# Kernel tuning notes

Measured on AMD Instinct MI355X. Metric: run time of the kernel, lower is better.

Reference implementation:

```python
import jax, jax.numpy as jnp
import numpy as np

B, L = 1, 768
D_MSA, D_PAIR, D_STATE, D_RBF = 256, 128, 16, 64
D_NODE, D_EDGE, L0_OUT = 32, 32, 16
D_MSG = 64
N_L1_IN, N_L1_OUT = 3, 2
NTOTALDOFS = 10
TOP_K = 128
D_HID = 128


def _ln(x):
    m = x.mean(-1, keepdims=True)
    v = ((x - m) ** 2).mean(-1, keepdims=True)
    return (x - m) / jnp.sqrt(v + 1e-5)


def _rbf(D):
    # RoseTTAFold-style gaussian RBF of pairwise distances
    mu = jnp.linspace(2.0, 22.0, D_RBF)
    sigma = (22.0 - 2.0) / D_RBF
    return jnp.exp(-((D[..., None] - mu) / sigma) ** 2)


def setup_inputs() -> dict:
    key = jax.random.key(0)
    ks = jax.random.split(key, 48)
    ki = iter(range(48))

    def lin(shape):
        k = ks[next(ki)]
        return jax.random.normal(k, shape, jnp.float32) / np.sqrt(shape[0]).astype(np.float32)

    inp = {
        'msa': jax.random.normal(ks[next(ki)], (B, 1, L, D_MSA), jnp.float32),
        'pair': jax.random.normal(ks[next(ki)], (B, L, L, D_PAIR), jnp.float32),
        'xyz': jax.random.normal(ks[next(ki)], (B, L, 3, 3), jnp.float32),
        'state': jax.random.normal(ks[next(ki)], (B, L, D_STATE), jnp.float32),
        'idx': jnp.tile(jnp.arange(L)[None, :], (B, 1)),
        'rotation_mask': jnp.zeros((B, L), bool),
        # node/edge embedding
        'W_en': lin((D_MSA + D_STATE, D_NODE)), 'b_en': jnp.zeros((D_NODE,)),
        'Wn1': lin((D_NODE, 2 * D_NODE)), 'bn1': jnp.zeros((2 * D_NODE,)),
        'Wn2': lin((2 * D_NODE, D_NODE)), 'bn2': jnp.zeros((D_NODE,)),
        'W_ee': lin((D_PAIR + D_RBF + 1, D_EDGE)), 'b_ee': jnp.zeros((D_EDGE,)),
        'We1': lin((D_EDGE, 2 * D_EDGE)), 'be1': jnp.zeros((2 * D_EDGE,)),
        'We2': lin((2 * D_EDGE, D_EDGE)), 'be2': jnp.zeros((D_EDGE,)),
        # SE3 message passing
        'Wm1': lin((2 * D_NODE + D_EDGE, D_MSG)), 'bm1': jnp.zeros((D_MSG,)),
        'Wm2': lin((D_MSG, D_NODE + N_L1_OUT + N_L1_OUT * N_L1_IN)),
        'bm2': jnp.zeros((D_NODE + N_L1_OUT + N_L1_OUT * N_L1_IN,)),
        'Wl0': lin((2 * D_NODE, L0_OUT)), 'bl0': jnp.zeros((L0_OUT,)),
        # SCPred
        'Ws0': lin((D_MSA, D_HID)), 'bs0': jnp.zeros((D_HID,)),
        'Wsi': lin((L0_OUT, D_HID)), 'bsi': jnp.zeros((D_HID,)),
        'Wp1': lin((D_HID, D_HID)), 'bp1': jnp.zeros((D_HID,)),
        'Wp2': lin((D_HID, D_HID)), 'bp2': jnp.zeros((D_HID,)),
        'Wp3': lin((D_HID, D_HID)), 'bp3': jnp.zeros((D_HID,)),
        'Wp4': lin((D_HID, D_HID)), 'bp4': jnp.zeros((D_HID,)),
        'Wout': lin((D_HID, 2 * NTOTALDOFS)), 'bout': jnp.zeros((2 * NTOTALDOFS,)),
    }
    return inp


def _forward(msa, pair, xyz, state, idx, rotation_mask,
             W_en, b_en, Wn1, bn1, Wn2, bn2, W_ee, b_ee, We1, be1, We2, be2,
             Wm1, bm1, Wm2, bm2, Wl0, bl0,
             Ws0, bs0, Wsi, bsi, Wp1, bp1, Wp2, bp2, Wp3, bp3, Wp4, bp4, Wout, bout):
    Bb, Ll = msa.shape[0], msa.shape[2]
    seq = _ln(msa[:, 0])                         # (B,L,d_msa)
    pair_n = _ln(pair)
    state_n = _ln(state)

    node = jnp.concatenate([seq, state_n], -1) @ W_en + b_en  # (B,L,32)
    node = node + jax.nn.relu(_ln(node) @ Wn1 + bn1) @ Wn2 + bn2
    node = _ln(node)

    # sequence-separation feature (B,L,L,1)
    off = (idx[:, None, :] - idx[:, :, None]).astype(jnp.float32)
    neighbor = (jnp.sign(off) * jnp.log(jnp.abs(off) + 1.0))[..., None]

    cas = xyz[:, :, 1]                            # (B,L,3) CA coords
    D = jnp.sqrt(jnp.sum((cas[:, :, None] - cas[:, None, :]) ** 2, -1) + 1e-8)
    rbf_feat = _rbf(D)                            # (B,L,L,64)

    edge = jnp.concatenate([pair_n, rbf_feat, neighbor], -1) @ W_ee + b_ee  # (B,L,L,32)
    edge = edge + jax.nn.relu(_ln(edge) @ We1 + be1) @ We2 + be2
    edge = _ln(edge)

    # top-k neighbor graph
    _, nbr = jax.lax.top_k(-D, TOP_K)             # (B,L,K)
    edge_feats = jnp.take_along_axis(edge, nbr[..., None], axis=2)  # (B,L,K,32)
    h_j = jax.vmap(lambda n, i: n[i])(node, nbr)                     # (B,L,K,32)
    x_j = jax.vmap(lambda c, i: c[i])(cas, nbr)                      # (B,L,K,3)
    h_i = jnp.broadcast_to(node[:, :, None, :], h_j.shape)

    # SE3-equivariant message passing (scalar messages + equivariant vector mixing)
    m_in = jnp.concatenate([h_i, h_j, edge_feats], -1)               # (B,L,K,96)
    m = jax.nn.relu(m_in @ Wm1 + bm1) @ Wm2 + bm2                    # (B,L,K,40)
    m_l0 = m[..., :D_NODE].mean(2)                                   # (B,L,32)
    w_edge = m[..., D_NODE:D_NODE + N_L1_OUT]                        # (B,L,K,2)
    w_atom = m[..., D_NODE + N_L1_OUT:].mean(2).reshape(Bb, Ll, N_L1_OUT, N_L1_IN)

    state_out = jnp.concatenate([node, m_l0], -1) @ Wl0 + bl0        # (B,L,16)

    rel = x_j - cas[:, :, None, :]                                   # (B,L,K,3)
    vec_edge = jnp.einsum('blkc,blkd->blcd', w_edge, rel) / TOP_K    # (B,L,2,3)
    l1_feats = xyz - xyz[:, :, 1:2, :]                               # (B,L,3,3)
    vec_atom = jnp.einsum('blca,blad->blcd', w_atom, l1_feats)
    offset = vec_edge + vec_atom                                     # (B,L,2,3)

    T = offset[:, :, 0, :] / 10.0
    R = offset[:, :, 1, :] / 100.0
    Qnorm = jnp.sqrt(1.0 + jnp.sum(R * R, -1))
    qA = 1.0 / Qnorm
    qB, qC, qD = R[..., 0] / Qnorm, R[..., 1] / Qnorm, R[..., 2] / Qnorm
    row0 = jnp.stack([qA*qA+qB*qB-qC*qC-qD*qD, 2*qB*qC-2*qA*qD, 2*qB*qD+2*qA*qC], -1)
    row1 = jnp.stack([2*qB*qC+2*qA*qD, qA*qA-qB*qB+qC*qC-qD*qD, 2*qC*qD-2*qA*qB], -1)
    row2 = jnp.stack([2*qB*qD-2*qA*qC, 2*qC*qD+2*qA*qB, qA*qA-qB*qB-qC*qC+qD*qD], -1)
    Rout = jnp.stack([row0, row1, row2], -2)                         # (B,L,3,3)
    I3 = jnp.broadcast_to(jnp.eye(3, dtype=Rout.dtype), Rout.shape)
    Rout = jnp.where(rotation_mask[:, :, None, None], I3, Rout)

    v = xyz - xyz[:, :, 1:2, :]
    xyz_new = jnp.einsum('blij,blaj->blai', Rout, v) + xyz[:, :, 1:2, :] + T[:, :, None, :]

    # SCPred torsion head
    s0 = _ln(msa[:, 0])
    si_in = _ln(state_out)
    si = s0 @ Ws0 + bs0 + si_in @ Wsi + bsi
    si = si + jax.nn.relu(jax.nn.relu(si) @ Wp1 + bp1) @ Wp2 + bp2
    si = si + jax.nn.relu(jax.nn.relu(si) @ Wp3 + bp3) @ Wp4 + bp4
    alpha = (jax.nn.relu(si) @ Wout + bout).reshape(Bb, Ll, NTOTALDOFS, 2)

    return xyz_new, state_out, alpha


def reference(msa, pair, xyz, state, idx, rotation_mask,
              W_en, b_en, Wn1, bn1, Wn2, bn2, W_ee, b_ee, We1, be1, We2, be2,
              Wm1, bm1, Wm2, bm2, Wl0, bl0,
              Ws0, bs0, Wsi, bsi, Wp1, bp1, Wp2, bp2, Wp3, bp3, Wp4, bp4, Wout, bout):
    return _forward(msa, pair, xyz, state, idx, rotation_mask,
                    W_en, b_en, Wn1, bn1, Wn2, bn2, W_ee, b_ee, We1, be1, We2, be2,
                    Wm1, bm1, Wm2, bm2, Wl0, bl0,
                    Ws0, bs0, Wsi, bsi, Wp1, bp1, Wp2, bp2, Wp3, bp3, Wp4, bp4, Wout, bout)


if __name__ == '__main__':
    out = reference(**setup_inputs())
    print([o.shape for o in out])
```

## Files before the change

kernel.cpp:

```cpp
#include <hip/hip_runtime.h>
#include <hip/hip_bf16.h>

#define LL 768
#define TOPK 128

#define WS_SEQ  0
#define WS_NODE (WS_SEQ + LL*256)
#define WS_NBR  (WS_NODE + LL*32)
#define WS_SOUT (WS_NBR + LL*TOPK)
#define WS_CSEE (WS_SOUT + LL*16)
#define WS_PK   (WS_CSEE + 32)

typedef __attribute__((ext_vector_type(8))) short  bf16x8_t;
typedef __attribute__((ext_vector_type(4))) float  f32x4_t;
typedef __attribute__((ext_vector_type(4))) unsigned u32x4_t;

__device__ __forceinline__ unsigned bfpack(float a, float b) {
  unsigned ua = __float_as_uint(a);
  ua = (ua + 0x7fffu + ((ua >> 16) & 1u)) >> 16;
  unsigned ub = __float_as_uint(b);
  ub = (ub + 0x7fffu + ((ub >> 16) & 1u)) & 0xffff0000u;
  return ua | ub;
}
__device__ __forceinline__ float bflo(unsigned v) { return __uint_as_float(v << 16); }
__device__ __forceinline__ float bfhi(unsigned v) { return __uint_as_float(v & 0xffff0000u); }

__device__ __forceinline__ float block_sum_256(float v, float* red, int t) {
#pragma unroll
  for (int o = 32; o > 0; o >>= 1) v += __shfl_xor(v, o, 64);
  __syncthreads();
  if ((t & 63) == 0) red[t >> 6] = v;
  __syncthreads();
  return red[0] + red[1] + red[2] + red[3];
}
// ... 192 lines not shown
    const int lane6 = t & 63;
    for (int f = t >> 6; f < 34; f += 4) {
      const float* W; int N, krow0, ct;
      if (f < 4)       { W = We1;  N = 64; krow0 = 0;                    ct = f;        }
      else if (f < 8)  { W = We2;  N = 32; krow0 = ((f-4)>>1)*32;        ct = (f-4)&1;  }
      else if (f < 12) { W = Wm1;  N = 64; krow0 = 32;                   ct = f-8;      }
      else if (f < 16) { W = Wm1;  N = 64; krow0 = 64;                   ct = f-12;     }
      else if (f < 22) { W = Wm2;  N = 40; krow0 = ((f-16)/3)*32;        ct = (f-16)%3; }
      else if (f < 30) { W = W_ee; N = 32; krow0 = ((f-22)>>1)*32;       ct = (f-22)&1; }
      else             { W = W_ee; N = 32; krow0 = 128 + ((f-30)>>1)*32; ct = (f-30)&1; }
      const int cc = ct*16 + (lane6 & 15);
      const int kb = krow0 + ((lane6 >> 4) << 3);
#pragma unroll
      for (int d = 0; d < 4; ++d) {
        const int k = kb + 2*d;
        const float lo = (cc < N) ? W[k*N + cc]     : 0.f;
        const float hi = (cc < N) ? W[(k+1)*N + cc] : 0.f;
        pkws[f*256 + lane6*4 + d] = bfpack(lo, hi);
      }
    }
  }
}

__global__ __launch_bounds__(256, 4) void kernC(
    const float* __restrict__ pair, const float* __restrict__ xyz,
    const int* __restrict__ idx, const unsigned char* __restrict__ rmask,
    const float* __restrict__ W_ee, const float* __restrict__ b_ee,
    const float* __restrict__ colsum_ee,
    const float* __restrict__ be1, const float* __restrict__ be2,
    const float* __restrict__ Wm1, const float* __restrict__ bm1,
    const float* __restrict__ bm2,
    const float* __restrict__ Wl0, const float* __restrict__ bl0,
    const float* __restrict__ node, const int* __restrict__ nbr,
    const unsigned* __restrict__ pkws,
    float* __restrict__ soutf, float* __restrict__ out)
{
  const int i = blockIdx.x, t = threadIdx.x;
  const int lane = t & 63;
  const int wv = __builtin_amdgcn_readfirstlane(t >> 6);
  __shared__ unsigned Ab[128][17];
  __shared__ unsigned U[128*33];
  __shared__ unsigned nd[128][17];
  __shared__ int   jl[128];
  __shared__ float Dvv[128], xsepv[128];
  __shared__ float relv[128][3];
  __shared__ float ni[32];
  __shared__ float pmv[64], prsv[64];
  __shared__ float mA[128], sgA[128];
  __shared__ float P2[4][44];
  __shared__ float fin[44];

  if (t < 32) ni[t] = node[i*32 + t];
  {
    const int pp = t >> 1, hh2 = t & 1;
    const int jj = nbr[i*TOPK + pp];
    const float4* nr = (const float4*)(node + jj*32 + hh2*16);
    float4 a0 = nr[0], a1 = nr[1], a2 = nr[2], a3 = nr[3];
    unsigned* dst = &nd[pp][hh2*8];
    dst[0] = bfpack(a0.x, a0.y); dst[1] = bfpack(a0.z, a0.w);
    dst[2] = bfpack(a1.x, a1.y); dst[3] = bfpack(a1.z, a1.w);
    dst[4] = bfpack(a2.x, a2.y); dst[5] = bfpack(a2.z, a2.w);
    dst[6] = bfpack(a3.x, a3.y); dst[7] = bfpack(a3.z, a3.w);
    if (hh2 == 0) {
      jl[pp] = jj;
      const float cix = xyz[i*9+3], ciy = xyz[i*9+4], ciz = xyz[i*9+5];
      const float cjx = xyz[jj*9+3], cjy = xyz[jj*9+4], cjz = xyz[jj*9+5];
      relv[pp][0] = cjx - cix;
      relv[pp][1] = cjy - ciy;
      relv[pp][2] = cjz - ciz;
      const float dx = __fadd_rn(cix, -cjx), dy = __fadd_rn(ciy, -cjy),
                  dz = __fadd_rn(ciz, -cjz);
      Dvv[pp] = sqrtf(__fadd_rn(__fadd_rn(__fadd_rn(__fmul_rn(dx,dx),
                        __fmul_rn(dy,dy)), __fmul_rn(dz,dz)), 1e-8f));
      const float offv = (float)(idx[jj] - idx[i]);
      const float sg = (offv > 0.f) ? 1.f : ((offv < 0.f) ? -1.f : 0.f);
      xsepv[pp] = sg * logf(fabsf(offv) + 1.f);
    }
  }
  __syncthreads();

  unsigned (*pairB)[65] = (unsigned (*)[65])U;
  const f32x4_t fz = {0.f, 0.f, 0.f, 0.f};
  for (int sub = 0; sub < 2; ++sub) {
    {
      const int r = t >> 2, qq = t & 3;
      const float* prow = pair + ((size_t)i*LL + jl[sub*64 + r])*128 + qq*32;
      float s = 0.f, ss = 0.f;
#pragma unroll
      for (int n = 0; n < 8; ++n) {
        float4 v = ((const float4*)prow)[n];
        s  += (v.x + v.y) + (v.z + v.w);
        ss += v.x*v.x + v.y*v.y + v.z*v.z + v.w*v.w;
        pairB[r][qq*16 + n*2]     = bfpack(v.x, v.y);
        pairB[r][qq*16 + n*2 + 1] = bfpack(v.z, v.w);
      }
      s  += __shfl_xor(s, 1);  s  += __shfl_xor(s, 2);
      ss += __shfl_xor(ss, 1); ss += __shfl_xor(ss, 2);
      if (qq == 0) {
        const float pm = s * (1.f/128.f);
        const float pv = ss * (1.f/128.f) - pm*pm;
        pmv[r] = pm; prsv[r] = 1.f / sqrtf(pv + 1e-5f);
      }
    }
    __syncthreads();
    {
      const int col = lane & 15, rg = lane >> 4;
      const int eM = wv*16;
      f32x4_t accP[2] = {fz, fz}, accR[2] = {fz, fz};
#pragma unroll
      for (int ks = 0; ks < 4; ++ks) {
        u32x4_t av;
        const unsigned* rp = &pairB[eM + col][ks*16 + rg*4];
        av.x = rp[0]; av.y = rp[1]; av.z = rp[2]; av.w = rp[3];
        const bf16x8_t af = __builtin_bit_cast(bf16x8_t, av);
#pragma unroll
        for (int ct = 0; ct < 2; ++ct) {
          const u32x4_t bv = ((const u32x4_t*)(pkws + (22 + ks*2 + ct)*256))[lane];
          accP[ct] = __builtin_amdgcn_mfma_f32_16x16x32_bf16(
              af, __builtin_bit_cast(bf16x8_t, bv), accP[ct], 0, 0, 0);
        }
      }
      const float Dv = Dvv[sub*64 + eM + col];
#pragma unroll
      for (int ks = 0; ks < 2; ++ks) {
        u32x4_t av;
#pragma unroll
        for (int d = 0; d < 4; ++d) {
          const int k = ks*32 + rg*8 + 2*d;
          const float mu0 = 2.f + (float)k     * (20.f/63.f);
          const float mu1 = 2.f + (float)(k+1) * (20.f/63.f);
          const float u0 = (Dv - mu0) / 0.3125f;
          const float u1 = (Dv - mu1) / 0.3125f;
          ((unsigned*)&av)[d] = bfpack(expf(-(u0*u0)), expf(-(u1*u1)));
        }
        const bf16x8_t af = __builtin_bit_cast(bf16x8_t, av);
#pragma unroll
        for (int ct = 0; ct < 2; ++ct) {
          const u32x4_t bv = ((const u32x4_t*)(pkws + (30 + ks*2 + ct)*256))[lane];
          accR[ct] = __builtin_amdgcn_mfma_f32_16x16x32_bf16(
              af, __builtin_bit_cast(bf16x8_t, bv), accR[ct], 0, 0, 0);
        }
      }
#pragma unroll
      for (int ct = 0; ct < 2; ++ct) {
        const int ch = ct*16 + col;
        const float cs = colsum_ee[ch];
        const float w3 = W_ee[192*32 + ch];
        const float bb = b_ee[ch];
#pragma unroll
        for (int j = 0; j < 4; ++j) {
          const int eloc = eM + rg*4 + j;
          const int e = sub*64 + eloc;
          const float prs = prsv[eloc], pm = pmv[eloc];
          float v = fmaf(prs, accP[ct][j],
                     fmaf(-prs*pm, cs,
                       fmaf(xsepv[e], w3, bb + accR[ct][j])));
          const float p = __shfl_xor(v, 1);
          if (!(lane & 1)) Ab[e][ct*8 + (col >> 1)] = bfpack(v, p);
        }
      }
    }
    __syncthreads();
  }

  unsigned (*Bb)[33] = (unsigned (*)[33])U;
  {
    const int e0b = 32 * wv;
    const int row = lane & 15;
    const int kg  = lane >> 4;
    const int r0  = kg * 4;

    {
      const int eL = e0b + (lane & 31);
      const int hf = lane >> 5;
      float av[16];
#pragma unroll
      for (int kk = 0; kk < 8; ++kk) {
        const unsigned v = Ab[eL][hf*8 + kk];
        av[2*kk] = bflo(v); av[2*kk+1] = bfhi(v);
      }
      float s = 0.f;
#pragma unroll
      for (int c = 0; c < 16; ++c) s += av[c];
      s += __shfl_xor(s, 32);
      const float mm = s * (1.f/32.f);
      float vv = 0.f;
#pragma unroll
      for (int c = 0; c < 16; ++c) { const float dd = av[c] - mm; vv += dd*dd; }
      vv += __shfl_xor(vv, 32);
      vv *= (1.f/32.f);
      const float sg = sqrtf(vv + 1e-5f);
      const float rs = 1.f / sg;
#pragma unroll
      for (int kk = 0; kk < 8; ++kk)
        Ab[eL][hf*8 + kk] = bfpack((av[2*kk]-mm)*rs, (av[2*kk+1]-mm)*rs);
      if (hf == 0) { mA[eL] = mm; sgA[eL] = sg; }
    }

    {
      f32x4_t acc[2][4];
#pragma unroll
      for (int m = 0; m < 2; ++m) {
        u32x4_t av4;
        const unsigned* rp = &Ab[e0b + 16*m + row][0];
        av4.x = rp[kg*4]; av4.y = rp[kg*4+1]; av4.z = rp[kg*4+2]; av4.w = rp[kg*4+3];
        const bf16x8_t af = __builtin_bit_cast(bf16x8_t, av4);
#pragma unroll
        for (int ct = 0; ct < 4; ++ct) {
          const u32x4_t bv = ((const u32x4_t*)(pkws + (0 + ct)*256))[lane];
          acc[m][ct] = __builtin_amdgcn_mfma_f32_16x16x32_bf16(
              af, __builtin_bit_cast(bf16x8_t, bv), fz, 0, 0, 0);
        }
      }
#pragma unroll
      for (int m = 0; m < 2; ++m)
#pragma unroll
        for (int ct = 0; ct < 4; ++ct) {
          const int ch = ct*16 + row;
#pragma unroll
          for (int j = 0; j < 4; ++j) {
            float v = fmaxf(acc[m][ct][j] + be1[ch], 0.f);
            const float p = __shfl_xor(v, 1);
            if (!(lane & 1))
              Bb[e0b + 16*m + r0 + j][ct*8 + (row >> 1)] = bfpack(v, p);
          }
        }
    }

    {
      f32x4_t acc[2][2];
#pragma unroll
      for (int m = 0; m < 2; ++m)
#pragma unroll
        for (int ct = 0; ct < 2; ++ct) acc[m][ct] = fz;
#pragma unroll
      for (int m = 0; m < 2; ++m)
#pragma unroll
        for (int ks = 0; ks < 2; ++ks) {
          u32x4_t av4;
          const unsigned* rp = &Bb[e0b + 16*m + row][0];
          const int kd = ks*16 + kg*4;
          av4.x = rp[kd]; av4.y = rp[kd+1]; av4.z = rp[kd+2]; av4.w = rp[kd+3];
          const bf16x8_t af = __builtin_bit_cast(bf16x8_t, av4);
#pragma unroll
          for (int ct = 0; ct < 2; ++ct) {
            const u32x4_t bv = ((const u32x4_t*)(pkws + (4 + ks*2 + ct)*256))[lane];
            acc[m][ct] = __builtin_amdgcn_mfma_f32_16x16x32_bf16(
                af, __builtin_bit_cast(bf16x8_t, bv), acc[m][ct], 0, 0, 0);
          }
        }
#pragma unroll
      for (int m = 0; m < 2; ++m)
#pragma unroll
        for (int ct = 0; ct < 2; ++ct) {
          const int ch = ct*16 + row;
          const int dw = ct*8 + (row >> 1);
#pragma unroll
          for (int j = 0; j < 4; ++j) {
            const int e = e0b + 16*m + r0 + j;
            const unsigned old = Ab[e][dw];
            const float e0v = (lane & 1) ? bfhi(old) : bflo(old);
            float v = acc[m][ct][j] + fmaf(e0v, sgA[e], mA[e]) + be2[ch];
            const float p = __shfl_xor(v, 1);
            if (!(lane & 1)) Ab[e][dw] = bfpack(v, p);
          }
        }
    }

    {
      const int eL = e0b + (lane & 31);
      const int hf = lane >> 5;
      float av[16];
#pragma unroll
      for (int kk = 0; kk < 8; ++kk) {
        const unsigned v = Ab[eL][hf*8 + kk];
        av[2*kk] = bflo(v); av[2*kk+1] = bfhi(v);
      }
      float s = 0.f;
#pragma unroll
      for (int c = 0; c < 16; ++c) s += av[c];
      s += __shfl_xor(s, 32);
      const float mm = s * (1.f/32.f);
      float vv = 0.f;
#pragma unroll
      for (int c = 0; c < 16; ++c) { const float dd = av[c] - mm; vv += dd*dd; }
      vv += __shfl_xor(vv, 32);
      vv *= (1.f/32.f);
      const float rs = 1.f / sqrtf(vv + 1e-5f);
#pragma unroll
      for (int kk = 0; kk < 8; ++kk)
        Ab[eL][hf*8 + kk] = bfpack((av[2*kk]-mm)*rs, (av[2*kk+1]-mm)*rs);
    }

    {
      float tmpni = bm1[lane];
      for (int k = 0; k < 32; ++k) tmpni = fmaf(ni[k], Wm1[k*64 + lane], tmpni);
      f32x4_t acc[2][4];
#pragma unroll
      for (int m = 0; m < 2; ++m)
#pragma unroll
        for (int ct = 0; ct < 4; ++ct) acc[m][ct] = fz;
#pragma unroll
      for (int m = 0; m < 2; ++m) {
        u32x4_t aN, aE;
        const unsigned* rn = &nd[e0b + 16*m + row][0];
        aN.x = rn[kg*4]; aN.y = rn[kg*4+1]; aN.z = rn[kg*4+2]; aN.w = rn[kg*4+3];
        const unsigned* ra = &Ab[e0b + 16*m + row][0];
        aE.x = ra[kg*4]; aE.y = ra[kg*4+1]; aE.z = ra[kg*4+2]; aE.w = ra[kg*4+3];
        const bf16x8_t afN = __builtin_bit_cast(bf16x8_t, aN);
        const bf16x8_t afE = __builtin_bit_cast(bf16x8_t, aE);
#pragma unroll
        for (int ct = 0; ct < 4; ++ct) {
          const u32x4_t bN = ((const u32x4_t*)(pkws + (8 + ct)*256))[lane];
          const u32x4_t bE = ((const u32x4_t*)(pkws + (12 + ct)*256))[lane];
          acc[m][ct] = __builtin_amdgcn_mfma_f32_16x16x32_bf16(
              afN, __builtin_bit_cast(bf16x8_t, bN), acc[m][ct], 0, 0, 0);
          acc[m][ct] = __builtin_amdgcn_mfma_f32_16x16x32_bf16(
              afE, __builtin_bit_cast(bf16x8_t, bE), acc[m][ct], 0, 0, 0);
        }
      }
#pragma unroll
      for (int m = 0; m < 2; ++m)
#pragma unroll
        for (int ct = 0; ct < 4; ++ct) {
          const int ch = ct*16 + row;
          const float tb = __shfl(tmpni, ch);
#pragma unroll
          for (int j = 0; j < 4; ++j) {
            float v = fmaxf(acc[m][ct][j] + tb, 0.f);
            const float p = __shfl_xor(v, 1);
            if (!(lane & 1))
              Bb[e0b + 16*m + r0 + j][ct*8 + (row >> 1)] = bfpack(v, p);
          }
        }
    }

    {
      f32x4_t acc[2][3];
#pragma unroll
      for (int m = 0; m < 2; ++m)
#pragma unroll
        for (int ct = 0; ct < 3; ++ct) acc[m][ct] = fz;
#pragma unroll
      for (int m = 0; m < 2; ++m)
#pragma unroll
        for (int ks = 0; ks < 2; ++ks) {
          u32x4_t av4;
          const unsigned* rp = &Bb[e0b + 16*m + row][0];
          const int kd = ks*16 + kg*4;
          av4.x = rp[kd]; av4.y = rp[kd+1]; av4.z = rp[kd+2]; av4.w = rp[kd+3];
          const bf16x8_t af = __builtin_bit_cast(bf16x8_t, av4);
#pragma unroll
          for (int ct = 0; ct < 3; ++ct) {
            const u32x4_t bv = ((const u32x4_t*)(pkws + (16 + ks*3 + ct)*256))[lane];
            acc[m][ct] = __builtin_amdgcn_mfma_f32_16x16x32_bf16(
                af, __builtin_bit_cast(bf16x8_t, bv), acc[m][ct], 0, 0, 0);
          }
        }
      float plain[3] = {0.f, 0.f, 0.f};
      float rel3[3]  = {0.f, 0.f, 0.f};
#pragma unroll
      for (int m = 0; m < 2; ++m)
#pragma unroll
        for (int ct = 0; ct < 3; ++ct) {
          const int o = ct*16 + row;
          if (ct == 2 && row >= 8) continue;
#pragma unroll
          for (int j = 0; j < 4; ++j) {
            const int e = e0b + 16*m + r0 + j;
            const float v = acc[m][ct][j] + bm2[o];
            if (ct == 2 && row < 2) {
              rel3[0] = fmaf(v, relv[e][0], rel3[0]);
              rel3[1] = fmaf(v, relv[e][1], rel3[1]);
              rel3[2] = fmaf(v, relv[e][2], rel3[2]);
            } else {
              plain[ct] += v;
            }
          }
        }
#pragma unroll
      for (int d = 0; d < 3; ++d) {
        plain[d] += __shfl_xor(plain[d], 16); plain[d] += __shfl_xor(plain[d], 32);
        rel3[d]  += __shfl_xor(rel3[d], 16);  rel3[d]  += __shfl_xor(rel3[d], 32);
      }
      if (lane < 16) {
        P2[wv][lane]      = plain[0];
        P2[wv][16 + lane] = plain[1];
        if (lane < 2) {
#pragma unroll
          for (int d = 0; d < 3; ++d) P2[wv][32 + lane*3 + d] = rel3[d];
        } else if (lane < 8) {
          P2[wv][38 + lane - 2] = plain[2];
        }
      }
    }
  }
  __syncthreads();
  if (t < 44) fin[t] = P2[0][t] + P2[1][t] + P2[2][t] + P2[3][t];
  __syncthreads();

  if (t < 16) {
    float a = bl0[t];
#pragma unroll
    for (int k = 0; k < 32; ++k) a = fmaf(ni[k], Wl0[k*16 + t], a);
#pragma unroll
    for (int k = 0; k < 32; ++k) a = fmaf(fin[k] * (1.f/128.f), Wl0[(32+k)*16 + t], a);
    soutf[i*16 + t] = a;
    out[LL*9 + i*16 + t] = a;
  }
  if (t == 0) {
    float ve[6], wa[6];
#pragma unroll
    for (int qq = 0; qq < 6; ++qq) ve[qq] = fin[32 + qq] * (1.f/128.f);
#pragma unroll
    for (int qq = 0; qq < 6; ++qq) wa[qq] = fin[38 + qq] * (1.f/128.f);
    float l1[9];
#pragma unroll
    for (int a = 0; a < 3; ++a)
#pragma unroll
      for (int d = 0; d < 3; ++d) l1[a*3 + d] = xyz[i*9 + a*3 + d] - xyz[i*9 + 3 + d];
    float T[3], Rv[3];
#pragma unroll
    for (int d = 0; d < 3; ++d) {
      float va0 = wa[0]*l1[d] + wa[1]*l1[3 + d] + wa[2]*l1[6 + d];
      float va1 = wa[3]*l1[d] + wa[4]*l1[3 + d] + wa[5]*l1[6 + d];
      T[d]  = (ve[d] + va0) / 10.f;
      Rv[d] = (ve[3 + d] + va1) / 100.f;
    }
    float qn = sqrtf(1.f + Rv[0]*Rv[0] + Rv[1]*Rv[1] + Rv[2]*Rv[2]);
    float qA = 1.f/qn, qB = Rv[0]/qn, qC = Rv[1]/qn, qD = Rv[2]/qn;
    float Rm[9];
    Rm[0] = qA*qA + qB*qB - qC*qC - qD*qD;
    Rm[1] = 2.f*qB*qC - 2.f*qA*qD;
    Rm[2] = 2.f*qB*qD + 2.f*qA*qC;
    Rm[3] = 2.f*qB*qC + 2.f*qA*qD;
    Rm[4] = qA*qA - qB*qB + qC*qC - qD*qD;
    Rm[5] = 2.f*qC*qD - 2.f*qA*qB;
    Rm[6] = 2.f*qB*qD - 2.f*qA*qC;
    Rm[7] = 2.f*qC*qD + 2.f*qA*qB;
    Rm[8] = qA*qA - qB*qB - qC*qC + qD*qD;
    if (rmask[i]) {
      Rm[0] = 1.f; Rm[1] = 0.f; Rm[2] = 0.f;
      Rm[3] = 0.f; Rm[4] = 1.f; Rm[5] = 0.f;
      Rm[6] = 0.f; Rm[7] = 0.f; Rm[8] = 1.f;
    }
#pragma unroll
    for (int a = 0; a < 3; ++a)
#pragma unroll
      for (int di = 0; di < 3; ++di) {
        float xn = Rm[di*3+0]*l1[a*3+0] + Rm[di*3+1]*l1[a*3+1] + Rm[di*3+2]*l1[a*3+2]
                 + xyz[i*9 + 3 + di] + T[di];
        out[i*9 + a*3 + di] = xn;
      }
  }
}

__global__ __launch_bounds__(512) void kernD(
    const float* __restrict__ seq_ln, const float* __restrict__ st_out,
    const float* __restrict__ Ws0, const float* __restrict__ bs0,
    const float* __restrict__ Wsi, const float* __restrict__ bsi,
    const float* __restrict__ Wp1, const float* __restrict__ bp1,
    const float* __restrict__ Wp2, const float* __restrict__ bp2,
    const float* __restrict__ Wp3, const float* __restrict__ bp3,
    const float* __restrict__ Wp4, const float* __restrict__ bp4,
    const float* __restrict__ Wout, const float* __restrict__ bout,
    float* __restrict__ out)
{
  const int i = blockIdx.x, t = threadIdx.x;
  const int c = t & 127, g = t >> 7;
  __shared__ float x0[256], stn[16], act[128], resid[128], part[4][129];

  if (t < 256) x0[t] = seq_ln[i*256 + t];
  if (t < 16) {
    float m = 0.f;
    for (int k = 0; k < 16; ++k) m += st_out[i*16 + k];
    m *= (1.f/16.f);
    float v = 0.f;
    for (int k = 0; k < 16; ++k) { float dd = st_out[i*16 + k] - m; v += dd*dd; }
    v *= (1.f/16.f);
    stn[t] = (st_out[i*16 + t] - m) / sqrtf(v + 1e-5f);
  }
  __syncthreads();

  {
    float p = 0.f;
    for (int k = g*64; k < g*64 + 64; ++k) p = fmaf(x0[k], Ws0[k*128 + c], p);
    if (g == 0)
      for (int k = 0; k < 16; ++k) p = fmaf(stn[k], Wsi[k*128 + c], p);
    part[g][c] = p;
  }
  __syncthreads();
  if (t < 128) {
    const float si = part[0][t] + part[1][t] + part[2][t] + part[3][t]
                   + bs0[t] + bsi[t];
    resid[t] = si;
    act[t] = fmaxf(si, 0.f);
  }
  __syncthreads();

  {
    float p = 0.f;
    for (int k = g*32; k < g*32 + 32; ++k) p = fmaf(act[k], Wp1[k*128 + c], p);
    part[g][c] = p;
// ... 71 lines not shown
  const float* Wm2  = (const float*)d_in[20];
  const float* bm2  = (const float*)d_in[21];
  const float* Wl0  = (const float*)d_in[22];
  const float* bl0  = (const float*)d_in[23];
  const float* Ws0  = (const float*)d_in[24];
  const float* bs0  = (const float*)d_in[25];
  const float* Wsi  = (const float*)d_in[26];
  const float* bsi  = (const float*)d_in[27];
  const float* Wp1  = (const float*)d_in[28];
  const float* bp1  = (const float*)d_in[29];
  const float* Wp2  = (const float*)d_in[30];
  const float* bp2  = (const float*)d_in[31];
  const float* Wp3  = (const float*)d_in[32];
  const float* bp3  = (const float*)d_in[33];
  const float* Wp4  = (const float*)d_in[34];
  const float* bp4  = (const float*)d_in[35];
  const float* Wout = (const float*)d_in[36];
  const float* bout = (const float*)d_in[37];

  float* wsf    = (float*)d_ws;
  float* seq_ln = wsf + WS_SEQ;
  float* nodev  = wsf + WS_NODE;
  int*   nbr    = (int*)(wsf + WS_NBR);
  float* soutf  = wsf + WS_SOUT;
  float* csee   = wsf + WS_CSEE;
  unsigned* pkws = (unsigned*)(wsf + WS_PK);
  float* out = (float*)d_out;

  kernABP<<<2*LL + 1, 256, 0, stream>>>(msa, state, W_en, b_en, Wn1, bn1, Wn2, bn2,
                                        xyz, W_ee, We1, We2, Wm1, Wm2,
                                        seq_ln, nodev, nbr, csee, pkws);
  kernC<<<LL, 256, 0, stream>>>(pair, xyz, idx, rmask, W_ee, b_ee, csee,
                                be1, be2, Wm1, bm1, bm2,
                                Wl0, bl0, nodev, nbr, pkws, soutf, out);
  kernD<<<LL, 512, 0, stream>>>(seq_ln, soutf, Ws0, bs0, Wsi, bsi, Wp1, bp1, Wp2, bp2,
                                Wp3, bp3, Wp4, bp4, Wout, bout, out);
}
```

Before: 81.73 us.

## Split kernC neighbor work across two blocks per residue and move finalization into kernD

kernC now runs two blocks per residue, each handling 64 of the 128 neighbors. Each block writes its partial message sums to a workspace buffer, and the per-residue state/xyz finalization moves into kernD, which adds the two partials. This doubles the grid, shrinks shared memory per block and raises the occupancy hint to 5, which should hide latency of the pair gathers better. The cost is an extra global round trip for the partials, and the per-block node-load and setup work is now duplicated.

New measurement: 73.96 us. -9.5%, faster.

```diff
diff --git a/kernel.cpp b/kernel.cpp
--- a/kernel.cpp
+++ b/kernel.cpp
@@ -7,9 +7,9 @@
 #define WS_SEQ  0
 #define WS_NODE (WS_SEQ + LL*256)
 #define WS_NBR  (WS_NODE + LL*32)
-#define WS_SOUT (WS_NBR + LL*TOPK)
-#define WS_CSEE (WS_SOUT + LL*16)
-#define WS_PK   (WS_CSEE + 32)
+#define WS_CSEE (WS_NBR + LL*TOPK)
+#define WS_FIN  (WS_CSEE + 32)
+#define WS_PK   (WS_FIN + LL*2*44)
 
 typedef __attribute__((ext_vector_type(8))) short  bf16x8_t;
 typedef __attribute__((ext_vector_type(4))) float  f32x4_t;
@@ -248,38 +248,35 @@
   }
 }
 
-__global__ __launch_bounds__(256, 4) void kernC(
+__global__ __launch_bounds__(256, 5) void kernC(
     const float* __restrict__ pair, const float* __restrict__ xyz,
-    const int* __restrict__ idx, const unsigned char* __restrict__ rmask,
+    const int* __restrict__ idx,
     const float* __restrict__ W_ee, const float* __restrict__ b_ee,
     const float* __restrict__ colsum_ee,
     const float* __restrict__ be1, const float* __restrict__ be2,
     const float* __restrict__ Wm1, const float* __restrict__ bm1,
     const float* __restrict__ bm2,
-    const float* __restrict__ Wl0, const float* __restrict__ bl0,
     const float* __restrict__ node, const int* __restrict__ nbr,
-    const unsigned* __restrict__ pkws,
-    float* __restrict__ soutf, float* __restrict__ out)
+    const unsigned* __restrict__ pkws, float* __restrict__ fin2)
 {
-  const int i = blockIdx.x, t = threadIdx.x;
-  const int lane = t & 63;
+  const int i = blockIdx.x >> 1, part = blockIdx.x & 1;
+  const int t = threadIdx.x, lane = t & 63;
   const int wv = __builtin_amdgcn_readfirstlane(t >> 6);
-  __shared__ unsigned Ab[128][17];
-  __shared__ unsigned U[128*33];
-  __shared__ unsigned nd[128][17];
-  __shared__ int   jl[128];
-  __shared__ float Dvv[128], xsepv[128];
-  __shared__ float relv[128][3];
+  __shared__ unsigned Ab[64][17];
+  __shared__ unsigned U[64*65];
+  __shared__ unsigned nd[64][17];
+  __shared__ int   jl[64];
+  __shared__ float Dvv[64], xsepv[64];
+  __shared__ float relv[64][3];
   __shared__ float ni[32];
   __shared__ float pmv[64], prsv[64];
-  __shared__ float mA[128], sgA[128];
+  __shared__ float mA[64], sgA[64];
   __shared__ float P2[4][44];
-  __shared__ float fin[44];
 
   if (t < 32) ni[t] = node[i*32 + t];
-  {
+  if (t < 128) {
     const int pp = t >> 1, hh2 = t & 1;
-    const int jj = nbr[i*TOPK + pp];
+    const int jj = nbr[i*TOPK + part*64 + pp];
     const float4* nr = (const float4*)(node + jj*32 + hh2*16);
     float4 a0 = nr[0], a1 = nr[1], a2 = nr[2], a3 = nr[3];
     unsigned* dst = &nd[pp][hh2*8];
@@ -306,304 +303,271 @@
   __syncthreads();
 
   unsigned (*pairB)[65] = (unsigned (*)[65])U;
+  {
+    const int r = t >> 2, qq = t & 3;
+    const float* prow = pair + ((size_t)i*LL + jl[r])*128 + qq*32;
+    float s = 0.f, ss = 0.f;
+#pragma unroll
+    for (int n = 0; n < 8; ++n) {
+      float4 v = ((const float4*)prow)[n];
+      s  += (v.x + v.y) + (v.z + v.w);
+      ss += v.x*v.x + v.y*v.y + v.z*v.z + v.w*v.w;
+      pairB[r][qq*16 + n*2]     = bfpack(v.x, v.y);
+      pairB[r][qq*16 + n*2 + 1] = bfpack(v.z, v.w);
+    }
+    s  += __shfl_xor(s, 1);  s  += __shfl_xor(s, 2);
+    ss += __shfl_xor(ss, 1); ss += __shfl_xor(ss, 2);
+    if (qq == 0) {
+      const float pm = s * (1.f/128.f);
+      const float pv = ss * (1.f/128.f) - pm*pm;
+      pmv[r] = pm; prsv[r] = 1.f / sqrtf(pv + 1e-5f);
+    }
+  }
+  __syncthreads();
+
   const f32x4_t fz = {0.f, 0.f, 0.f, 0.f};
-  for (int sub = 0; sub < 2; ++sub) {
-    {
-      const int r = t >> 2, qq = t & 3;
-      const float* prow = pair + ((size_t)i*LL + jl[sub*64 + r])*128 + qq*32;
-      float s = 0.f, ss = 0.f;
-#pragma unroll
-      for (int n = 0; n < 8; ++n) {
-        float4 v = ((const float4*)prow)[n];
-        s  += (v.x + v.y) + (v.z + v.w);
-        ss += v.x*v.x + v.y*v.y + v.z*v.z + v.w*v.w;
-        pairB[r][qq*16 + n*2]     = bfpack(v.x, v.y);
-        pairB[r][qq*16 + n*2 + 1] = bfpack(v.z, v.w);
-      }
-      s  += __shfl_xor(s, 1);  s  += __shfl_xor(s, 2);
-      ss += __shfl_xor(ss, 1); ss += __shfl_xor(ss, 2);
-      if (qq == 0) {
-        const float pm = s * (1.f/128.f);
-        const float pv = ss * (1.f/128.f) - pm*pm;
-        pmv[r] = pm; prsv[r] = 1.f / sqrtf(pv + 1e-5f);
-      }
-    }
-    __syncthreads();
-    {
-      const int col = lane & 15, rg = lane >> 4;
-      const int eM = wv*16;
-      f32x4_t accP[2] = {fz, fz}, accR[2] = {fz, fz};
-#pragma unroll
-      for (int ks = 0; ks < 4; ++ks) {
-        u32x4_t av;
-        const unsigned* rp = &pairB[eM + col][ks*16 + rg*4];
-        av.x = rp[0]; av.y = rp[1]; av.z = rp[2]; av.w = rp[3];
-        const bf16x8_t af = __builtin_bit_cast(bf16x8_t, av);
-#pragma unroll
-        for (int ct = 0; ct < 2; ++ct) {
-          const u32x4_t bv = ((const u32x4_t*)(pkws + (22 + ks*2 + ct)*256))[lane];
-          accP[ct] = __builtin_amdgcn_mfma_f32_16x16x32_bf16(
-              af, __builtin_bit_cast(bf16x8_t, bv), accP[ct], 0, 0, 0);
-        }
-      }
-      const float Dv = Dvv[sub*64 + eM + col];
-#pragma unroll
-      for (int ks = 0; ks < 2; ++ks) {
-        u32x4_t av;
-#pragma unroll
-        for (int d = 0; d < 4; ++d) {
-          const int k = ks*32 + rg*8 + 2*d;
-          const float mu0 = 2.f + (float)k     * (20.f/63.f);
-          const float mu1 = 2.f + (float)(k+1) * (20.f/63.f);
-          const float u0 = (Dv - mu0) / 0.3125f;
-          const float u1 = (Dv - mu1) / 0.3125f;
-          ((unsigned*)&av)[d] = bfpack(expf(-(u0*u0)), expf(-(u1*u1)));
-        }
-        const bf16x8_t af = __builtin_bit_cast(bf16x8_t, av);
-#pragma unroll
-        for (int ct = 0; ct < 2; ++ct) {
-          const u32x4_t bv = ((const u32x4_t*)(pkws + (30 + ks*2 + ct)*256))[lane];
-          accR[ct] = __builtin_amdgcn_mfma_f32_16x16x32_bf16(
-              af, __builtin_bit_cast(bf16x8_t, bv), accR[ct], 0, 0, 0);
-        }
-      }
+
+  {
+    const int col = lane & 15, rg = lane >> 4;
+    const int eM = wv*16;
+    f32x4_t accP[2] = {fz, fz}, accR[2] = {fz, fz};
+#pragma unroll
+    for (int ks = 0; ks < 4; ++ks) {
+      u32x4_t av;
+      const unsigned* rp = &pairB[eM + col][ks*16 + rg*4];
+      av.x = rp[0]; av.y = rp[1]; av.z = rp[2]; av.w = rp[3];
+      const bf16x8_t af = __builtin_bit_cast(bf16x8_t, av);
 #pragma unroll
       for (int ct = 0; ct < 2; ++ct) {
-        const int ch = ct*16 + col;
-        const float cs = colsum_ee[ch];
-        const float w3 = W_ee[192*32 + ch];
-        const float bb = b_ee[ch];
-#pragma unroll
-        for (int j = 0; j < 4; ++j) {
-          const int eloc = eM + rg*4 + j;
-          const int e = sub*64 + eloc;
-          const float prs = prsv[eloc], pm = pmv[eloc];
-          float v = fmaf(prs, accP[ct][j],
-                     fmaf(-prs*pm, cs,
-                       fmaf(xsepv[e], w3, bb + accR[ct][j])));
-          const float p = __shfl_xor(v, 1);
-          if (!(lane & 1)) Ab[e][ct*8 + (col >> 1)] = bfpack(v, p);
-        }
-      }
-    }
-    __syncthreads();
-  }
+        const u32x4_t bv = ((const u32x4_t*)(pkws + (22 + ks*2 + ct)*256))[lane];
+        accP[ct] = __builtin_amdgcn_mfma_f32_16x16x32_bf16(
+            af, __builtin_bit_cast(bf16x8_t, bv), accP[ct], 0, 0, 0);
+      }
+    }
+    const float Dv = Dvv[eM + col];
+#pragma unroll
+    for (int ks = 0; ks < 2; ++ks) {
+      u32x4_t av;
+#pragma unroll
+      for (int d = 0; d < 4; ++d) {
+        const int k = ks*32 + rg*8 + 2*d;
+        const float mu0 = 2.f + (float)k     * (20.f/63.f);
+        const float mu1 = 2.f + (float)(k+1) * (20.f/63.f);
+        const float u0 = (Dv - mu0) / 0.3125f;
+        const float u1 = (Dv - mu1) / 0.3125f;
+        ((unsigned*)&av)[d] = bfpack(expf(-(u0*u0)), expf(-(u1*u1)));
+      }
+      const bf16x8_t af = __builtin_bit_cast(bf16x8_t, av);
+#pragma unroll
+      for (int ct = 0; ct < 2; ++ct) {
+        const u32x4_t bv = ((const u32x4_t*)(pkws + (30 + ks*2 + ct)*256))[lane];
+        accR[ct] = __builtin_amdgcn_mfma_f32_16x16x32_bf16(
+            af, __builtin_bit_cast(bf16x8_t, bv), accR[ct], 0, 0, 0);
+      }
+    }
+#pragma unroll
+    for (int ct = 0; ct < 2; ++ct) {
+      const int ch = ct*16 + col;
+      const float cs = colsum_ee[ch];
+      const float w3 = W_ee[192*32 + ch];
+      const float bb = b_ee[ch];
+#pragma unroll
+      for (int j = 0; j < 4; ++j) {
+        const int e = eM + rg*4 + j;
+        const float prs = prsv[e], pm = pmv[e];
+        float v = fmaf(prs, accP[ct][j],
+                   fmaf(-prs*pm, cs,
+                     fmaf(xsepv[e], w3, bb + accR[ct][j])));
+        const float p = __shfl_xor(v, 1);
+        if (!(lane & 1)) Ab[e][ct*8 + (col >> 1)] = bfpack(v, p);
+      }
+    }
+  }
+  __syncthreads();
 
   unsigned (*Bb)[33] = (unsigned (*)[33])U;
   {
-    const int e0b = 32 * wv;
+    const int e0b = 16 * wv;
     const int row = lane & 15;
     const int kg  = lane >> 4;
     const int r0  = kg * 4;
 
     {
-      const int eL = e0b + (lane & 31);
-      const int hf = lane >> 5;
-      float av[16];
-#pragma unroll
-      for (int kk = 0; kk < 8; ++kk) {
-        const unsigned v = Ab[eL][hf*8 + kk];
+      const int eL = e0b + row;
+      float av[8];
+#pragma unroll
+      for (int kk = 0; kk < 4; ++kk) {
+        const unsigned v = Ab[eL][kg*4 + kk];
         av[2*kk] = bflo(v); av[2*kk+1] = bfhi(v);
       }
       float s = 0.f;
 #pragma unroll
-      for (int c = 0; c < 16; ++c) s += av[c];
-      s += __shfl_xor(s, 32);
+      for (int c = 0; c < 8; ++c) s += av[c];
+      s += __shfl_xor(s, 16); s += __shfl_xor(s, 32);
       const float mm = s * (1.f/32.f);
       float vv = 0.f;
 #pragma unroll
-      for (int c = 0; c < 16; ++c) { const float dd = av[c] - mm; vv += dd*dd; }
-      vv += __shfl_xor(vv, 32);
+      for (int c = 0; c < 8; ++c) { const float dd = av[c] - mm; vv += dd*dd; }
+      vv += __shfl_xor(vv, 16); vv += __shfl_xor(vv, 32);
       vv *= (1.f/32.f);
       const float sg = sqrtf(vv + 1e-5f);
       const float rs = 1.f / sg;
 #pragma unroll
-      for (int kk = 0; kk < 8; ++kk)
-        Ab[eL][hf*8 + kk] = bfpack((av[2*kk]-mm)*rs, (av[2*kk+1]-mm)*rs);
-      if (hf == 0) { mA[eL] = mm; sgA[eL] = sg; }
+      for (int kk = 0; kk < 4; ++kk)
+        Ab[eL][kg*4 + kk] = bfpack((av[2*kk]-mm)*rs, (av[2*kk+1]-mm)*rs);
+      if (kg == 0) { mA[eL] = mm; sgA[eL] = sg; }
     }
 
     {
-      f32x4_t acc[2][4];
-#pragma unroll
-      for (int m = 0; m < 2; ++m) {
+      u32x4_t av4;
+      const unsigned* rp = &Ab[e0b + row][0];
+      av4.x = rp[kg*4]; av4.y = rp[kg*4+1]; av4.z = rp[kg*4+2]; av4.w = rp[kg*4+3];
+      const bf16x8_t af = __builtin_bit_cast(bf16x8_t, av4);
+      f32x4_t acc[4];
+#pragma unroll
+      for (int ct = 0; ct < 4; ++ct) {
+        const u32x4_t bv = ((const u32x4_t*)(pkws + (0 + ct)*256))[lane];
+        acc[ct] = __builtin_amdgcn_mfma_f32_16x16x32_bf16(
+            af, __builtin_bit_cast(bf16x8_t, bv), fz, 0, 0, 0);
+      }
+#pragma unroll
+      for (int ct = 0; ct < 4; ++ct) {
+        const int ch = ct*16 + row;
+#pragma unroll
+        for (int j = 0; j < 4; ++j) {
+          float v = fmaxf(acc[ct][j] + be1[ch], 0.f);
+          const float p = __shfl_xor(v, 1);
+          if (!(lane & 1))
+            Bb[e0b + r0 + j][ct*8 + (row >> 1)] = bfpack(v, p);
+        }
+      }
+    }
+
+    {
+      f32x4_t acc[2] = {fz, fz};
+#pragma unroll
+      for (int ks = 0; ks < 2; ++ks) {
         u32x4_t av4;
-        const unsigned* rp = &Ab[e0b + 16*m + row][0];
-        av4.x = rp[kg*4]; av4.y = rp[kg*4+1]; av4.z = rp[kg*4+2]; av4.w = rp[kg*4+3];
+        const unsigned* rp = &Bb[e0b + row][0];
+        const int kd = ks*16 + kg*4;
+        av4.x = rp[kd]; av4.y = rp[kd+1]; av4.z = rp[kd+2]; av4.w = rp[kd+3];
         const bf16x8_t af = __builtin_bit_cast(bf16x8_t, av4);
 #pragma unroll
-        for (int ct = 0; ct < 4; ++ct) {
-          const u32x4_t bv = ((const u32x4_t*)(pkws + (0 + ct)*256))[lane];
-          acc[m][ct] = __builtin_amdgcn_mfma_f32_16x16x32_bf16(
-              af, __builtin_bit_cast(bf16x8_t, bv), fz, 0, 0, 0);
+        for (int ct = 0; ct < 2; ++ct) {
+          const u32x4_t bv = ((const u32x4_t*)(pkws + (4 + ks*2 + ct)*256))[lane];
+          acc[ct] = __builtin_amdgcn_mfma_f32_16x16x32_bf16(
+              af, __builtin_bit_cast(bf16x8_t, bv), acc[ct], 0, 0, 0);
         }
       }
 #pragma unroll
-      for (int m = 0; m < 2; ++m)
-#pragma unroll
-        for (int ct = 0; ct < 4; ++ct) {
-          const int ch = ct*16 + row;
-#pragma unroll
-          for (int j = 0; j < 4; ++j) {
-            float v = fmaxf(acc[m][ct][j] + be1[ch], 0.f);
-            const float p = __shfl_xor(v, 1);
-            if (!(lane & 1))
-              Bb[e0b + 16*m + r0 + j][ct*8 + (row >> 1)] = bfpack(v, p);
-          }
+      for (int ct = 0; ct < 2; ++ct) {
+        const int ch = ct*16 + row;
+        const int dw = ct*8 + (row >> 1);
+#pragma unroll
+        for (int j = 0; j < 4; ++j) {
+          const int e = e0b + r0 + j;
+          const unsigned old = Ab[e][dw];
+          const float e0v = (lane & 1) ? bfhi(old) : bflo(old);
+          float v = acc[ct][j] + fmaf(e0v, sgA[e], mA[e]) + be2[ch];
+          const float p = __shfl_xor(v, 1);
+          if (!(lane & 1)) Ab[e][dw] = bfpack(v, p);
         }
+      }
     }
 
     {
-      f32x4_t acc[2][2];
-#pragma unroll
-      for (int m = 0; m < 2; ++m)
-#pragma unroll
-        for (int ct = 0; ct < 2; ++ct) acc[m][ct] = fz;
-#pragma unroll
-      for (int m = 0; m < 2; ++m)
-#pragma unroll
-        for (int ks = 0; ks < 2; ++ks) {
-          u32x4_t av4;
-          const unsigned* rp = &Bb[e0b + 16*m + row][0];
-          const int kd = ks*16 + kg*4;
-          av4.x = rp[kd]; av4.y = rp[kd+1]; av4.z = rp[kd+2]; av4.w = rp[kd+3];
-          const bf16x8_t af = __builtin_bit_cast(bf16x8_t, av4);
-#pragma unroll
-          for (int ct = 0; ct < 2; ++ct) {
-            const u32x4_t bv = ((const u32x4_t*)(pkws + (4 + ks*2 + ct)*256))[lane];
-            acc[m][ct] = __builtin_amdgcn_mfma_f32_16x16x32_bf16(
-                af, __builtin_bit_cast(bf16x8_t, bv), acc[m][ct], 0, 0, 0);
-          }
-        }
-#pragma unroll
-      for (int m = 0; m < 2; ++m)
-#pragma unroll
-        for (int ct = 0; ct < 2; ++ct) {
-          const int ch = ct*16 + row;
-          const int dw = ct*8 + (row >> 1);
-#pragma unroll
-          for (int j = 0; j < 4; ++j) {
-            const int e = e0b + 16*m + r0 + j;
-            const unsigned old = Ab[e][dw];
-            const float e0v = (lane & 1) ? bfhi(old) : bflo(old);
-            float v = acc[m][ct][j] + fmaf(e0v, sgA[e], mA[e]) + be2[ch];
-            const float p = __shfl_xor(v, 1);
-            if (!(lane & 1)) Ab[e][dw] = bfpack(v, p);
-          }
-        }
-    }
-
-    {
-      const int eL = e0b + (lane & 31);
-      const int hf = lane >> 5;
-      float av[16];
-#pragma unroll
-      for (int kk = 0; kk < 8; ++kk) {
-        const unsigned v = Ab[eL][hf*8 + kk];
+      const int eL = e0b + row;
+      float av[8];
+#pragma unroll
+      for (int kk = 0; kk < 4; ++kk) {
+        const unsigned v = Ab[eL][kg*4 + kk];
         av[2*kk] = bflo(v); av[2*kk+1] = bfhi(v);
       }
       float s = 0.f;
 #pragma unroll
-      for (int c = 0; c < 16; ++c) s += av[c];
-      s += __shfl_xor(s, 32);
+      for (int c = 0; c < 8; ++c) s += av[c];
+      s += __shfl_xor(s, 16); s += __shfl_xor(s, 32);
       const float mm = s * (1.f/32.f);
       float vv = 0.f;
 #pragma unroll
-      for (int c = 0; c < 16; ++c) { const float dd = av[c] - mm; vv += dd*dd; }
-      vv += __shfl_xor(vv, 32);
+      for (int c = 0; c < 8; ++c) { const float dd = av[c] - mm; vv += dd*dd; }
+      vv += __shfl_xor(vv, 16); vv += __shfl_xor(vv, 32);
       vv *= (1.f/32.f);
       const float rs = 1.f / sqrtf(vv + 1e-5f);
 #pragma unroll
-      for (int kk = 0; kk < 8; ++kk)
-        Ab[eL][hf*8 + kk] = bfpack((av[2*kk]-mm)*rs, (av[2*kk+1]-mm)*rs);
+      for (int kk = 0; kk < 4; ++kk)
+        Ab[eL][kg*4 + kk] = bfpack((av[2*kk]-mm)*rs, (av[2*kk+1]-mm)*rs);
     }
 
     {
       float tmpni = bm1[lane];
       for (int k = 0; k < 32; ++k) tmpni = fmaf(ni[k], Wm1[k*64 + lane], tmpni);
-      f32x4_t acc[2][4];
-#pragma unroll
-      for (int m = 0; m < 2; ++m)
-#pragma unroll
-        for (int ct = 0; ct < 4; ++ct) acc[m][ct] = fz;
-#pragma unroll
-      for (int m = 0; m < 2; ++m) {
-        u32x4_t aN, aE;
-        const unsigned* rn = &nd[e0b + 16*m + row][0];
-        aN.x = rn[kg*4]; aN.y = rn[kg*4+1]; aN.z = rn[kg*4+2]; aN.w = rn[kg*4+3];
-        const unsigned* ra = &Ab[e0b + 16*m + row][0];
-        aE.x = ra[kg*4]; aE.y = ra[kg*4+1]; aE.z = ra[kg*4+2]; aE.w = ra[kg*4+3];
-        const bf16x8_t afN = __builtin_bit_cast(bf16x8_t, aN);
-        const bf16x8_t afE = __builtin_bit_cast(bf16x8_t, aE);
-#pragma unroll
-        for (int ct = 0; ct < 4; ++ct) {
-          const u32x4_t bN = ((const u32x4_t*)(pkws + (8 + ct)*256))[lane];
-          const u32x4_t bE = ((const u32x4_t*)(pkws + (12 + ct)*256))[lane];
-          acc[m][ct] = __builtin_amdgcn_mfma_f32_16x16x32_bf16(
-              afN, __builtin_bit_cast(bf16x8_t, bN), acc[m][ct], 0, 0, 0);
-          acc[m][ct] = __builtin_amdgcn_mfma_f32_16x16x32_bf16(
-              afE, __builtin_bit_cast(bf16x8_t, bE), acc[m][ct], 0, 0, 0);
+      u32x4_t aN, aE;
+      const unsigned* rn = &nd[e0b + row][0];
+      aN.x = rn[kg*4]; aN.y = rn[kg*4+1]; aN.z = rn[kg*4+2]; aN.w = rn[kg*4+3];
+      const unsigned* ra = &Ab[e0b + row][0];
+      aE.x = ra[kg*4]; aE.y = ra[kg*4+1]; aE.z = ra[kg*4+2]; aE.w = ra[kg*4+3];
+      const bf16x8_t afN = __builtin_bit_cast(bf16x8_t, aN);
+      const bf16x8_t afE = __builtin_bit_cast(bf16x8_t, aE);
+      f32x4_t acc[4];
+#pragma unroll
+      for (int ct = 0; ct < 4; ++ct) {
+        const u32x4_t bN = ((const u32x4_t*)(pkws + (8 + ct)*256))[lane];
+        const u32x4_t bE = ((const u32x4_t*)(pkws + (12 + ct)*256))[lane];
+        acc[ct] = __builtin_amdgcn_mfma_f32_16x16x32_bf16(
+            afN, __builtin_bit_cast(bf16x8_t, bN), fz, 0, 0, 0);
+        acc[ct] = __builtin_amdgcn_mfma_f32_16x16x32_bf16(
+            afE, __builtin_bit_cast(bf16x8_t, bE), acc[ct], 0, 0, 0);
+      }
+#pragma unroll
+      for (int ct = 0; ct < 4; ++ct) {
+        const int ch = ct*16 + row;
+        const float tb = __shfl(tmpni, ch);
+#pragma unroll
+        for (int j = 0; j < 4; ++j) {
+          float v = fmaxf(acc[ct][j] + tb, 0.f);
+          const float p = __shfl_xor(v, 1);
+          if (!(lane & 1))
+            Bb[e0b + r0 + j][ct*8 + (row >> 1)] = bfpack(v, p);
         }
       }
-#pragma unroll
-      for (int m = 0; m < 2; ++m)
-#pragma unroll
-        for (int ct = 0; ct < 4; ++ct) {
-          const int ch = ct*16 + row;
-          const float tb = __shfl(tmpni, ch);
-#pragma unroll
-          for (int j = 0; j < 4; ++j) {
-            float v = fmaxf(acc[m][ct][j] + tb, 0.f);
-            const float p = __shfl_xor(v, 1);
-            if (!(lane & 1))
-              Bb[e0b + 16*m + r0 + j][ct*8 + (row >> 1)] = bfpack(v, p);
+    }
+
+    {
+      f32x4_t acc[3] = {fz, fz, fz};
+#pragma unroll
+      for (int ks = 0; ks < 2; ++ks) {
+        u32x4_t av4;
+        const unsigned* rp = &Bb[e0b + row][0];
+        const int kd = ks*16 + kg*4;
+        av4.x = rp[kd]; av4.y = rp[kd+1]; av4.z = rp[kd+2]; av4.w = rp[kd+3];
+        const bf16x8_t af = __builtin_bit_cast(bf16x8_t, av4);
+#pragma unroll
+        for (int ct = 0; ct < 3; ++ct) {
+          const u32x4_t bv = ((const u32x4_t*)(pkws + (16 + ks*3 + ct)*256))[lane];
+          acc[ct] = __builtin_amdgcn_mfma_f32_16x16x32_bf16(
+              af, __builtin_bit_cast(bf16x8_t, bv), acc[ct], 0, 0, 0);
+        }
+      }
+      float plain[3] = {0.f, 0.f, 0.f};
+      float rel3[3]  = {0.f, 0.f, 0.f};
+#pragma unroll
+      for (int ct = 0; ct < 3; ++ct) {
+        const int o = ct*16 + row;
+        if (ct == 2 && row >= 8) continue;
+#pragma unroll
+        for (int j = 0; j < 4; ++j) {
+          const int e = e0b + r0 + j;
+          const float v = acc[ct][j] + bm2[o];
+          if (ct == 2 && row < 2) {
+            rel3[0] = fmaf(v, relv[e][0], rel3[0]);
+            rel3[1] = fmaf(v, relv[e][1], rel3[1]);
+            rel3[2] = fmaf(v, relv[e][2], rel3[2]);
+          } else {
+            plain[ct] += v;
           }
         }
-    }
-
-    {
-      f32x4_t acc[2][3];
-#pragma unroll
-      for (int m = 0; m < 2; ++m)
-#pragma unroll
-        for (int ct = 0; ct < 3; ++ct) acc[m][ct] = fz;
-#pragma unroll
-      for (int m = 0; m < 2; ++m)
-#pragma unroll
-        for (int ks = 0; ks < 2; ++ks) {
-          u32x4_t av4;
-          const unsigned* rp = &Bb[e0b + 16*m + row][0];
-          const int kd = ks*16 + kg*4;
-          av4.x = rp[kd]; av4.y = rp[kd+1]; av4.z = rp[kd+2]; av4.w = rp[kd+3];
-          const bf16x8_t af = __builtin_bit_cast(bf16x8_t, av4);
-#pragma unroll
-          for (int ct = 0; ct < 3; ++ct) {
-            const u32x4_t bv = ((const u32x4_t*)(pkws + (16 + ks*3 + ct)*256))[lane];
-            acc[m][ct] = __builtin_amdgcn_mfma_f32_16x16x32_bf16(
-                af, __builtin_bit_cast(bf16x8_t, bv), acc[m][ct], 0, 0, 0);
-          }
-        }
-      float plain[3] = {0.f, 0.f, 0.f};
-      float rel3[3]  = {0.f, 0.f, 0.f};
-#pragma unroll
-      for (int m = 0; m < 2; ++m)
-#pragma unroll
-        for (int ct = 0; ct < 3; ++ct) {
-          const int o = ct*16 + row;
-          if (ct == 2 && row >= 8) continue;
-#pragma unroll
-          for (int j = 0; j < 4; ++j) {
-            const int e = e0b + 16*m + r0 + j;
-            const float v = acc[m][ct][j] + bm2[o];
-            if (ct == 2 && row < 2) {
-              rel3[0] = fmaf(v, relv[e][0], rel3[0]);
-              rel3[1] = fmaf(v, relv[e][1], rel3[1]);
-              rel3[2] = fmaf(v, relv[e][2], rel3[2]);
-            } else {
-              plain[ct] += v;
-            }
-          }
-        }
+      }
 #pragma unroll
       for (int d = 0; d < 3; ++d) {
         plain[d] += __shfl_xor(plain[d], 16); plain[d] += __shfl_xor(plain[d], 32);
@@ -622,19 +586,45 @@
     }
   }
   __syncthreads();
-  if (t < 44) fin[t] = P2[0][t] + P2[1][t] + P2[2][t] + P2[3][t];
+  if (t < 44)
+    fin2[(size_t)(i*2 + part)*44 + t] = P2[0][t] + P2[1][t] + P2[2][t] + P2[3][t];
+}
+
+__global__ __launch_bounds__(512) void kernD(
+    const float* __restrict__ seq_ln, const float* __restrict__ xyz,
+    const unsigned char* __restrict__ rmask,
+    const float* __restrict__ Wl0, const float* __restrict__ bl0,
+    const float* __restrict__ node, const float* __restrict__ fin2,
+    const float* __restrict__ Ws0, const float* __restrict__ bs0,
+    const float* __restrict__ Wsi, const float* __restrict__ bsi,
+    const float* __restrict__ Wp1, const float* __restrict__ bp1,
+    const float* __restrict__ Wp2, const float* __restrict__ bp2,
+    const float* __restrict__ Wp3, const float* __restrict__ bp3,
+    const float* __restrict__ Wp4, const float* __restrict__ bp4,
+    const float* __restrict__ Wout, const float* __restrict__ bout,
+    float* __restrict__ out)
+{
+  const int i = blockIdx.x, t = threadIdx.x;
+  const int c = t & 127, g = t >> 7;
+  __shared__ float fin[44], niD[32], sout_s[16], stn[16];
+  __shared__ float x0[256], act[128], resid[128], part[4][129];
+
+  if (t < 44) fin[t] = fin2[(size_t)(i*2)*44 + t] + fin2[(size_t)(i*2+1)*44 + t];
+  if (t >= 64 && t < 96) niD[t-64] = node[i*32 + (t-64)];
+  if (t >= 256) x0[t-256] = seq_ln[i*256 + (t-256)];
+  else if (t >= 128) x0[t] = seq_ln[i*256 + t];
   __syncthreads();
 
   if (t < 16) {
     float a = bl0[t];
 #pragma unroll
-    for (int k = 0; k < 32; ++k) a = fmaf(ni[k], Wl0[k*16 + t], a);
+    for (int k = 0; k < 32; ++k) a = fmaf(niD[k], Wl0[k*16 + t], a);
 #pragma unroll
     for (int k = 0; k < 32; ++k) a = fmaf(fin[k] * (1.f/128.f), Wl0[(32+k)*16 + t], a);
-    soutf[i*16 + t] = a;
+    sout_s[t] = a;
     out[LL*9 + i*16 + t] = a;
   }
-  if (t == 0) {
+  if (t == 32) {
     float ve[6], wa[6];
 #pragma unroll
     for (int qq = 0; qq < 6; ++qq) ve[qq] = fin[32 + qq] * (1.f/128.f);
@@ -679,32 +669,16 @@
         out[i*9 + a*3 + di] = xn;
       }
   }
-}
-
-__global__ __launch_bounds__(512) void kernD(
-    const float* __restrict__ seq_ln, const float* __restrict__ st_out,
-    const float* __restrict__ Ws0, const float* __restrict__ bs0,
-    const float* __restrict__ Wsi, const float* __restrict__ bsi,
-    const float* __restrict__ Wp1, const float* __restrict__ bp1,
-    const float* __restrict__ Wp2, const float* __restrict__ bp2,
-    const float* __restrict__ Wp3, const float* __restrict__ bp3,
-    const float* __restrict__ Wp4, const float* __restrict__ bp4,
-    const float* __restrict__ Wout, const float* __restrict__ bout,
-    float* __restrict__ out)
-{
-  const int i = blockIdx.x, t = threadIdx.x;
-  const int c = t & 127, g = t >> 7;
-  __shared__ float x0[256], stn[16], act[128], resid[128], part[4][129];
-
-  if (t < 256) x0[t] = seq_ln[i*256 + t];
+  __syncthreads();
+
   if (t < 16) {
     float m = 0.f;
-    for (int k = 0; k < 16; ++k) m += st_out[i*16 + k];
+    for (int k = 0; k < 16; ++k) m += sout_s[k];
     m *= (1.f/16.f);
     float v = 0.f;
-    for (int k = 0; k < 16; ++k) { float dd = st_out[i*16 + k] - m; v += dd*dd; }
+    for (int k = 0; k < 16; ++k) { float dd = sout_s[k] - m; v += dd*dd; }
     v *= (1.f/16.f);
-    stn[t] = (st_out[i*16 + t] - m) / sqrtf(v + 1e-5f);
+    stn[t] = (sout_s[t] - m) / sqrtf(v + 1e-5f);
   }
   __syncthreads();
 
@@ -822,17 +796,18 @@
   float* seq_ln = wsf + WS_SEQ;
   float* nodev  = wsf + WS_NODE;
   int*   nbr    = (int*)(wsf + WS_NBR);
-  float* soutf  = wsf + WS_SOUT;
   float* csee   = wsf + WS_CSEE;
+  float* fin2   = wsf + WS_FIN;
   unsigned* pkws = (unsigned*)(wsf + WS_PK);
   float* out = (float*)d_out;
 
   kernABP<<<2*LL + 1, 256, 0, stream>>>(msa, state, W_en, b_en, Wn1, bn1, Wn2, bn2,
                                         xyz, W_ee, We1, We2, Wm1, Wm2,
                                         seq_ln, nodev, nbr, csee, pkws);
-  kernC<<<LL, 256, 0, stream>>>(pair, xyz, idx, rmask, W_ee, b_ee, csee,
-                                be1, be2, Wm1, bm1, bm2,
-                                Wl0, bl0, nodev, nbr, pkws, soutf, out);
-  kernD<<<LL, 512, 0, stream>>>(seq_ln, soutf, Ws0, bs0, Wsi, bsi, Wp1, bp1, Wp2, bp2,
+  kernC<<<2*LL, 256, 0, stream>>>(pair, xyz, idx, W_ee, b_ee, csee,
+                                  be1, be2, Wm1, bm1, bm2,
+                                  nodev, nbr, pkws, fin2);
+  kernD<<<LL, 512, 0, stream>>>(seq_ln, xyz, rmask, Wl0, bl0, nodev, fin2,
+                                Ws0, bs0, Wsi, bsi, Wp1, bp1, Wp2, bp2,
                                 Wp3, bp3, Wp4, bp4, Wout, bout, out);
 }
```
